# Kernel tuning notes

Hardware: AMD Instinct MI355X
Metric: run time of the kernel (lower is better)

Reference implementation:

```python
import jax, jax.numpy as jnp
import numpy as np

B, S, D_IN, D_H = 16, 4096, 512, 512

def setup_inputs() -> dict:
    key = jax.random.key(0)
    ks = jax.random.split(key, 8)
    inp = {
        "input": jax.random.normal(ks[0], (B, D_IN), dtype=jnp.float32),
        "context": jax.random.normal(ks[1], (B, S, D_IN), dtype=jnp.float32),
        "mask": jax.random.bernoulli(ks[2], 0.2, (B, S)),
        # parameters (torch nn.Linear layout: W [out,in], b [out])
        "W_in": jax.random.normal(ks[3], (D_H, D_IN), dtype=jnp.float32) / np.sqrt(D_IN),
        "b_in": jax.random.normal(ks[4], (D_H,), dtype=jnp.float32) * 0.01,
        "W_ctx": jax.random.normal(ks[5], (D_H, D_IN), dtype=jnp.float32) / np.sqrt(D_IN),
        "b_ctx": jax.random.normal(ks[6], (D_H,), dtype=jnp.float32) * 0.01,
        "v": jax.random.normal(ks[7], (D_H,), dtype=jnp.float32),
    }
    return inp


def reference(input, context, mask, W_in, b_in, W_ctx, b_ctx, v):
    # inp: [B, H] projected decoder state
    inp = input @ W_in.T + b_in
    # ctx: [B, S, H] projected context (this is what the torch code matmuls
    # with the softmax weights, i.e. hidden lives in hidden_dim space)
    ctx = context @ W_ctx.T + b_ctx
    # additive (Bahdanau) scores: v . tanh(inp + ctx) -> [B, S]
    scores = jnp.einsum("h,bsh->bs", v, jnp.tanh(inp[:, None, :] + ctx))
    # masked positions get -inf so they receive zero softmax weight
    scores = jnp.where(mask, -jnp.inf, scores)
    attn = jax.nn.softmax(scores, axis=-1)  # [B, S]
    # weighted sum of projected context: [B, H]
    hidden = jnp.einsum("bsh,bs->bh", ctx, attn)
    return hidden, attn
```

## Files before the change

kernel.cpp:

```cpp
#include <hip/hip_runtime.h>
#include <hip/hip_bf16.h>

#define B_  16
#define S_  4096
#define DIN 512
#define DH  512

typedef _Float16 f16x8 __attribute__((ext_vector_type(8)));
typedef float    f32x4 __attribute__((ext_vector_type(4)));


__device__ __forceinline__ float fast_tanh(float x) {
    float e = __expf(2.f * x);
    return 1.f - 2.f * __builtin_amdgcn_rcpf(e + 1.f);
}

__device__ __forceinline__ void gload_lds16(const void* g, void* l) {
    __builtin_amdgcn_global_load_lds(
        (const __attribute__((address_space(1))) void*)g,
        (__attribute__((address_space(3))) void*)l, 16, 0, 0);
}

__device__ __forceinline__ int mask_at(const void* mask, int isByte, int idx) {
    return isByte ? (int)((const unsigned char*)mask)[idx]
                  : ((const int*)mask)[idx];
}

__global__ __launch_bounds__(256)
void prep_kernel(const float* __restrict__ input,
                 const float* __restrict__ W_in,
                 const float* __restrict__ b_in,
                 const float* __restrict__ W_ctx,
                 const float* __restrict__ b_ctx,
                 const void*  __restrict__ mask,
                 _Float16* __restrict__ W16,
                 float* __restrict__ addv,
                 float* __restrict__ wsum,
                 int* __restrict__ maskflag) {
    int blk = blockIdx.x;
    int tid = threadIdx.x;
    if (blk < 256) {
        int base = blk * 1024 + tid * 4;
        float4 wv = *(const float4*)(W_ctx + base);
        union { _Float16 f[4]; ushort4 u; } cv;
        cv.f[0] = (_Float16)wv.x; cv.f[1] = (_Float16)wv.y;
        cv.f[2] = (_Float16)wv.z; cv.f[3] = (_Float16)wv.w;
        *(ushort4*)(W16 + base) = cv.u;
    } else if (blk < 288) {
        int t = blk - 256;
        int b = t >> 1;
        int h = ((t & 1) << 8) + tid;
        __shared__ float inrow[DIN];
        inrow[tid]       = input[b * DIN + tid];
        inrow[tid + 256] = input[b * DIN + tid + 256];
        __syncthreads();
        const float* wr = W_in + (size_t)h * DIN;
        float acc = 0.f;
        for (int k = 0; k < DIN; k += 4) {
            float4 w4 = *(const float4*)(wr + k);
            acc += w4.x * inrow[k] + w4.y * inrow[k + 1]
                 + w4.z * inrow[k + 2] + w4.w * inrow[k + 3];
        }
        addv[b * DH + h] = acc + b_in[h] + b_ctx[h];
    } else if (blk == 288) {
        const uint4* m4 = (const uint4*)mask;
        unsigned int orw = 0;
#pragma unroll
        for (int it = 0; it < 16; ++it) {
            uint4 w = m4[it * 256 + tid];
            orw |= (w.x | w.y | w.z | w.w);
        }
        int found = ((orw & 0xFFFFFF00u) != 0) ? 1 : 0;
        __shared__ int f;
        if (tid == 0) f = 0;
        __syncthreads();
        if (found) atomicOr(&f, 1);
        __syncthreads();
        if (tid == 0) maskflag[0] = f;
    } else {
        int base = (blk - 289) * 4096;
#pragma unroll
        for (int it = 0; it < 16; ++it)
            wsum[base + it * 256 + tid] = 0.f;
    }
}

__global__ __launch_bounds__(512, 1)
void score_kernel(const float* __restrict__ context,
                  const _Float16* __restrict__ W16,
                  const float* __restrict__ addv,
                  const float* __restrict__ v,
                  float* __restrict__ scores) {
    __shared__ __align__(16) _Float16 As[2][4096];
    __shared__ __align__(16) _Float16 Bs[2][16384];

    const int tid  = threadIdx.x;
    const int wave = tid >> 6;
    const int lane = tid & 63;
    const int l15  = lane & 15;
    const int q    = lane >> 4;
    const int sg   = wave >> 2;
    const int ng   = wave & 3;

    const int b  = blockIdx.x >> 5;
    const int st = blockIdx.x & 31;
    const int s0 = st * 128;

    const float* ctxA = context + ((size_t)b * S_ + s0) * DIN;

    const int rowA = ((tid >> 6) * 16) + (tid & 15);
    const int kbA  = ((tid >> 4) & 3) * 8;

#define STAGE_B(kc_, buf_)                                                     \
    {                                                                          \
        _Pragma("unroll")                                                      \
        for (int u = 0; u < 4; ++u) {                                          \
            int jn = wave * 4 + u;                                             \
            const _Float16* gp = W16 +                                         \
                (size_t)(jn * 16 + l15) * DIN + (kc_) * 32 + q * 8;            \
            gload_lds16(gp, &Bs[buf_][jn * 512]);                              \
        }                                                                      \
    }

#define LOADA(kc_, set_)                                                       \
    {                                                                          \
        const float* g0 = ctxA + (size_t)rowA * DIN + (kc_) * 32 + kbA;        \
        set_[0] = *(const float4*)g0;                                          \
        set_[1] = *(const float4*)(g0 + 4);                                    \
    }

#define WRITEA(set_, buf_)                                                     \
    {                                                                          \
        f16x8 h0;                                                              \
        h0[0] = (_Float16)set_[0].x; h0[1] = (_Float16)set_[0].y;              \
        h0[2] = (_Float16)set_[0].z; h0[3] = (_Float16)set_[0].w;              \
        h0[4] = (_Float16)set_[1].x; h0[5] = (_Float16)set_[1].y;              \
        h0[6] = (_Float16)set_[1].z; h0[7] = (_Float16)set_[1].w;              \
        *(f16x8*)&As[buf_][tid * 8] = h0;                                      \
    }

    f32x4 acc[4][8];
#pragma unroll
    for (int jm = 0; jm < 4; ++jm)
#pragma unroll
        for (int jn = 0; jn < 8; ++jn) acc[jm][jn] = (f32x4){0.f, 0.f, 0.f, 0.f};

    float4 aA[2], aB[2];

    STAGE_B(0, 0);
    LOADA(0, aA);
    WRITEA(aA, 0);
    LOADA(1, aB);
    __syncthreads();

#define STEP(kc_, buf_, ldset_, wrset_)                                        \
    {                                                                          \
        if ((kc_) + 1 < 16) STAGE_B((kc_) + 1, (buf_) ^ 1);                    \
        if ((kc_) + 2 < 16) LOADA((kc_) + 2, ldset_);                          \
        f16x8 afr[4], bfr[8];                                                  \
        _Pragma("unroll")                                                      \
        for (int jm = 0; jm < 4; ++jm)                                         \
            afr[jm] = *(const f16x8*)&As[buf_][(sg * 4 + jm) * 512 +           \
                                              q * 128 + l15 * 8];              \
        _Pragma("unroll")                                                      \
        for (int jn = 0; jn < 8; ++jn)                                         \
            bfr[jn] = *(const f16x8*)&Bs[buf_][(ng * 8 + jn) * 512 +           \
                                              q * 128 + l15 * 8];              \
        _Pragma("unroll")                                                      \
        for (int jn = 0; jn < 8; ++jn)                                         \
            _Pragma("unroll")                                                  \
            for (int jm = 0; jm < 4; ++jm)                                     \
                acc[jm][jn] = __builtin_amdgcn_mfma_f32_16x16x32_f16(          \
                    afr[jm], bfr[jn], acc[jm][jn], 0, 0, 0);                   \
        if ((kc_) + 1 < 16) WRITEA(wrset_, (buf_) ^ 1);                        \
        __syncthreads();                                                       \
    }

    for (int kp = 0; kp < 8; ++kp) {
        STEP(2 * kp,     0, aA, aB);
        STEP(2 * kp + 1, 1, aB, aA);
    }

    const float* avb = addv + b * DH;
    float rowsum[4][4] = {{0.f,0.f,0.f,0.f},{0.f,0.f,0.f,0.f},
                          {0.f,0.f,0.f,0.f},{0.f,0.f,0.f,0.f}};
#pragma unroll
    for (int jn = 0; jn < 8; ++jn) {
        int n = (ng * 8 + jn) * 16 + l15;
        float av = avb[n];
        float vv = v[n];
#pragma unroll
        for (int jm = 0; jm < 4; ++jm)
#pragma unroll
            for (int r = 0; r < 4; ++r)
                rowsum[jm][r] += vv * fast_tanh(acc[jm][jn][r] + av);
    }
    float* sredF = (float*)&As[0][0];
#pragma unroll
    for (int jm = 0; jm < 4; ++jm)
#pragma unroll
        for (int r = 0; r < 4; ++r) {
            float s = rowsum[jm][r];
            s += __shfl_xor(s, 1, 16);
            s += __shfl_xor(s, 2, 16);
            s += __shfl_xor(s, 4, 16);
            s += __shfl_xor(s, 8, 16);
            if (l15 == 0) {
                int rowL = (sg * 4 + jm) * 16 + q * 4 + r;
                sredF[ng * 128 + rowL] = s;
            }
        }
    __syncthreads();
    if (tid < 128) {
        float out = sredF[tid] + sredF[128 + tid] +
                    sredF[256 + tid] + sredF[384 + tid];
        scores[b * S_ + s0 + tid] = out;
    }
}

__global__ __launch_bounds__(256)
void attnwsum_kernel(const float* __restrict__ scores,
                     const float* __restrict__ context,
                     const void* __restrict__ mask,
                     const int* __restrict__ maskflag,
                     float* __restrict__ attn,
                     float* __restrict__ wsum) {
    __shared__ float rbuf[8];
    __shared__ int   selIdx[64];
    __shared__ float selW[64];
    __shared__ int   selCount;

    int b  = blockIdx.x >> 6;
    int c0 = (blockIdx.x & 63) * 64;
    int tid = threadIdx.x;
    int wv = tid >> 6, ln = tid & 63;
    int isByte = maskflag[0];
    const float* sr = scores + b * S_;

    float mx = -__builtin_inff();
    float vals[16];
#pragma unroll
    for (int it = 0; it < 16; ++it) {
        int s = it * 256 + tid;
        float x = mask_at(mask, isByte, b * S_ + s) ? -__builtin_inff() : sr[s];
        vals[it] = x;
        mx = fmaxf(mx, x);
    }
    for (int o = 1; o < 64; o <<= 1) mx = fmaxf(mx, __shfl_xor(mx, o, 64));
    if (ln == 0) rbuf[wv] = mx;
    __syncthreads();
    mx = fmaxf(fmaxf(rbuf[0], rbuf[1]), fmaxf(rbuf[2], rbuf[3]));

    float sum = 0.f;
#pragma unroll
    for (int it = 0; it < 16; ++it) sum += __expf(vals[it] - mx);
    for (int o = 1; o < 64; o <<= 1) sum += __shfl_xor(sum, o, 64);
    if (ln == 0) rbuf[4 + wv] = sum;
    if (tid == 0) selCount = 0;
    __syncthreads();
    float inv = 1.f / (rbuf[4] + rbuf[5] + rbuf[6] + rbuf[7]);

    if (tid < 64) {
        int s = c0 + tid;
        int idx = b * S_ + s;
        float sc = mask_at(mask, isByte, idx) ? -__builtin_inff() : sr[s];
        float p = __expf(sc - mx) * inv;
        attn[idx] = p;
        if (p > 1e-9f) {
            int k = atomicAdd(&selCount, 1);
            selIdx[k] = s;
            selW[k]  = p;
        }
    }
    __syncthreads();

    int cnt = selCount;
    if (cnt == 0) return;
    const float* cb = context + (size_t)b * S_ * DIN;
    float a00 = 0.f, a01 = 0.f, a10 = 0.f, a11 = 0.f;
    float a20 = 0.f, a21 = 0.f, a30 = 0.f, a31 = 0.f;
    int i = 0;
    for (; i + 4 <= cnt; i += 4) {
        const float* c0p = cb + (size_t)selIdx[i]     * DIN;
        const float* c1p = cb + (size_t)selIdx[i + 1] * DIN;
        const float* c2p = cb + (size_t)selIdx[i + 2] * DIN;
        const float* c3p = cb + (size_t)selIdx[i + 3] * DIN;
        float w0 = selW[i], w1 = selW[i + 1], w2 = selW[i + 2], w3 = selW[i + 3];
        a00 += w0 * c0p[tid]; a01 += w0 * c0p[tid + 256];
        a10 += w1 * c1p[tid]; a11 += w1 * c1p[tid + 256];
        a20 += w2 * c2p[tid]; a21 += w2 * c2p[tid + 256];
        a30 += w3 * c3p[tid]; a31 += w3 * c3p[tid + 256];
    }
    float acc0 = (a00 + a10) + (a20 + a30);
    float acc1 = (a01 + a11) + (a21 + a31);
    for (; i < cnt; ++i) {
        const float* cr = cb + (size_t)selIdx[i] * DIN;
        float w = selW[i];
        acc0 += w * cr[tid];
        acc1 += w * cr[tid + 256];
    }
    atomicAdd(&wsum[b * DIN + tid], acc0);
    atomicAdd(&wsum[b * DIN + tid + 256], acc1);
}

__global__ __launch_bounds__(256)
void hidden_kernel(const float* __restrict__ W_ctx,
                   const float* __restrict__ b_ctx,
                   const float* __restrict__ wsum,
                   float* __restrict__ hidden) {
    int b = blockIdx.x >> 1;
    int tid = threadIdx.x;
    int h = ((blockIdx.x & 1) << 8) + tid;
    __shared__ float wrow[DIN];
    wrow[tid]       = wsum[b * DIN + tid];
    wrow[tid + 256] = wsum[b * DIN + tid + 256];
    __syncthreads();
    const float* wr = W_ctx + (size_t)h * DIN;
    float acc = 0.f;
    for (int k = 0; k < DIN; k += 4) {
        float4 w4 = *(const float4*)(wr + k);
        acc += w4.x * wrow[k] + w4.y * wrow[k + 1]
             + w4.z * wrow[k + 2] + w4.w * wrow[k + 3];
    }
    hidden[b * DH + h] = acc + b_ctx[h];
}

extern "C" void kernel_launch(void* const* d_in, const int* in_sizes, int n_in,
                              void* d_out, int out_size, void* d_ws, size_t ws_size,
                              hipStream_t stream) {
    const float* input   = (const float*)d_in[0];
    const float* context = (const float*)d_in[1];
    const void*  mask    = d_in[2];
    const float* W_in    = (const float*)d_in[3];
    const float* b_in    = (const float*)d_in[4];
    const float* W_ctx   = (const float*)d_in[5];
    const float* b_ctx   = (const float*)d_in[6];
    const float* v       = (const float*)d_in[7];

    char* ws = (char*)d_ws;
    _Float16* W16   = (_Float16*)ws;
    float* addv     = (float*)(ws + 524288);
    float* scores   = (float*)(ws + 557056);
    float* wsum     = (float*)(ws + 819200);
    int*   maskflag = (int*)(ws + 851968);

    float* hidden = (float*)d_out;
    float* attn   = (float*)d_out + B_ * DH;

    prep_kernel<<<291, 256, 0, stream>>>(input, W_in, b_in, W_ctx, b_ctx, mask,
                                         W16, addv, wsum, maskflag);
    score_kernel<<<512, 512, 0, stream>>>(context, W16, addv, v, scores);
    attnwsum_kernel<<<B_ * 64, 256, 0, stream>>>(scores, context, mask, maskflag,
                                                 attn, wsum);
    hidden_kernel<<<B_ * 2, 256, 0, stream>>>(W_ctx, b_ctx, wsum, hidden);
}
```

Measured before the change: 290.4 us.

## Double score kernel waves to 1024 threads with halved per-wave row tiles

Launches the score GEMM with 16 waves per block instead of 8. Each wave now owns two 16-row M tiles instead of four, and context loading and W staging are re-split so each thread handles half as much. The aim is more waves in flight to hide global load latency on the context stream, plus lower per-wave register use. The cost is more LDS reads of B fragments, since each one is now shared by twice as many waves, and heavier barriers with 1024 threads.

```diff
diff --git a/kernel.cpp b/kernel.cpp
--- a/kernel.cpp
+++ b/kernel.cpp
@@ -7,6 +7,7 @@
 #define DH  512
 
 typedef _Float16 f16x8 __attribute__((ext_vector_type(8)));
+typedef _Float16 f16x4 __attribute__((ext_vector_type(4)));
 typedef float    f32x4 __attribute__((ext_vector_type(4)));
 
 
@@ -85,7 +86,7 @@
     }
 }
 
-__global__ __launch_bounds__(512, 1)
+__global__ __launch_bounds__(1024)
 void score_kernel(const float* __restrict__ context,
                   const _Float16* __restrict__ W16,
                   const float* __restrict__ addv,
@@ -108,14 +109,14 @@
 
     const float* ctxA = context + ((size_t)b * S_ + s0) * DIN;
 
-    const int rowA = ((tid >> 6) * 16) + (tid & 15);
-    const int kbA  = ((tid >> 4) & 3) * 8;
+    const int rowA = ((tid >> 7) * 16) + ((tid >> 1) & 15);
+    const int kbA  = (((tid >> 5) & 3) * 8) + ((tid & 1) * 4);
 
 #define STAGE_B(kc_, buf_)                                                     \
     {                                                                          \
         _Pragma("unroll")                                                      \
-        for (int u = 0; u < 4; ++u) {                                          \
-            int jn = wave * 4 + u;                                             \
+        for (int u = 0; u < 2; ++u) {                                          \
+            int jn = wave * 2 + u;                                             \
             const _Float16* gp = W16 +                                         \
                 (size_t)(jn * 16 + l15) * DIN + (kc_) * 32 + q * 8;            \
             gload_lds16(gp, &Bs[buf_][jn * 512]);                              \
@@ -124,28 +125,24 @@
 
 #define LOADA(kc_, set_)                                                       \
     {                                                                          \
-        const float* g0 = ctxA + (size_t)rowA * DIN + (kc_) * 32 + kbA;        \
-        set_[0] = *(const float4*)g0;                                          \
-        set_[1] = *(const float4*)(g0 + 4);                                    \
+        set_ = *(const float4*)(ctxA + (size_t)rowA * DIN + (kc_) * 32 + kbA); \
     }
 
 #define WRITEA(set_, buf_)                                                     \
     {                                                                          \
-        f16x8 h0;                                                              \
-        h0[0] = (_Float16)set_[0].x; h0[1] = (_Float16)set_[0].y;              \
-        h0[2] = (_Float16)set_[0].z; h0[3] = (_Float16)set_[0].w;              \
-        h0[4] = (_Float16)set_[1].x; h0[5] = (_Float16)set_[1].y;              \
-        h0[6] = (_Float16)set_[1].z; h0[7] = (_Float16)set_[1].w;              \
-        *(f16x8*)&As[buf_][tid * 8] = h0;                                      \
-    }
-
-    f32x4 acc[4][8];
-#pragma unroll
-    for (int jm = 0; jm < 4; ++jm)
+        f16x4 h0;                                                              \
+        h0[0] = (_Float16)set_.x; h0[1] = (_Float16)set_.y;                    \
+        h0[2] = (_Float16)set_.z; h0[3] = (_Float16)set_.w;                    \
+        *(f16x4*)&As[buf_][tid * 4] = h0;                                      \
+    }
+
+    f32x4 acc[2][8];
+#pragma unroll
+    for (int jm = 0; jm < 2; ++jm)
 #pragma unroll
         for (int jn = 0; jn < 8; ++jn) acc[jm][jn] = (f32x4){0.f, 0.f, 0.f, 0.f};
 
-    float4 aA[2], aB[2];
+    float4 aA, aB;
 
     STAGE_B(0, 0);
     LOADA(0, aA);
@@ -157,21 +154,20 @@
     {                                                                          \
         if ((kc_) + 1 < 16) STAGE_B((kc_) + 1, (buf_) ^ 1);                    \
         if ((kc_) + 2 < 16) LOADA((kc_) + 2, ldset_);                          \
-        f16x8 afr[4], bfr[8];                                                  \
+        f16x8 afr[2];                                                          \
         _Pragma("unroll")                                                      \
-        for (int jm = 0; jm < 4; ++jm)                                         \
-            afr[jm] = *(const f16x8*)&As[buf_][(sg * 4 + jm) * 512 +           \
+        for (int jm = 0; jm < 2; ++jm)                                         \
+            afr[jm] = *(const f16x8*)&As[buf_][(sg * 2 + jm) * 512 +           \
                                               q * 128 + l15 * 8];              \
         _Pragma("unroll")                                                      \
-        for (int jn = 0; jn < 8; ++jn)                                         \
-            bfr[jn] = *(const f16x8*)&Bs[buf_][(ng * 8 + jn) * 512 +           \
-                                              q * 128 + l15 * 8];              \
-        _Pragma("unroll")                                                      \
-        for (int jn = 0; jn < 8; ++jn)                                         \
-            _Pragma("unroll")                                                  \
-            for (int jm = 0; jm < 4; ++jm)                                     \
-                acc[jm][jn] = __builtin_amdgcn_mfma_f32_16x16x32_f16(          \
-                    afr[jm], bfr[jn], acc[jm][jn], 0, 0, 0);                   \
+        for (int jn = 0; jn < 8; ++jn) {                                       \
+            f16x8 bfr = *(const f16x8*)&Bs[buf_][(ng * 8 + jn) * 512 +         \
+                                                q * 128 + l15 * 8];            \
+            acc[0][jn] = __builtin_amdgcn_mfma_f32_16x16x32_f16(               \
+                afr[0], bfr, acc[0][jn], 0, 0, 0);                             \
+            acc[1][jn] = __builtin_amdgcn_mfma_f32_16x16x32_f16(               \
+                afr[1], bfr, acc[1][jn], 0, 0, 0);                             \
+        }                                                                      \
         if ((kc_) + 1 < 16) WRITEA(wrset_, (buf_) ^ 1);                        \
         __syncthreads();                                                       \
     }
@@ -182,22 +178,21 @@
     }
 
     const float* avb = addv + b * DH;
-    float rowsum[4][4] = {{0.f,0.f,0.f,0.f},{0.f,0.f,0.f,0.f},
-                          {0.f,0.f,0.f,0.f},{0.f,0.f,0.f,0.f}};
+    float rowsum[2][4] = {{0.f,0.f,0.f,0.f},{0.f,0.f,0.f,0.f}};
 #pragma unroll
     for (int jn = 0; jn < 8; ++jn) {
         int n = (ng * 8 + jn) * 16 + l15;
         float av = avb[n];
         float vv = v[n];
 #pragma unroll
-        for (int jm = 0; jm < 4; ++jm)
+        for (int jm = 0; jm < 2; ++jm)
 #pragma unroll
             for (int r = 0; r < 4; ++r)
                 rowsum[jm][r] += vv * fast_tanh(acc[jm][jn][r] + av);
     }
     float* sredF = (float*)&As[0][0];
 #pragma unroll
-    for (int jm = 0; jm < 4; ++jm)
+    for (int jm = 0; jm < 2; ++jm)
 #pragma unroll
         for (int r = 0; r < 4; ++r) {
             float s = rowsum[jm][r];
@@ -206,7 +201,7 @@
             s += __shfl_xor(s, 4, 16);
             s += __shfl_xor(s, 8, 16);
             if (l15 == 0) {
-                int rowL = (sg * 4 + jm) * 16 + q * 4 + r;
+                int rowL = (sg * 2 + jm) * 16 + q * 4 + r;
                 sredF[ng * 128 + rowL] = s;
             }
         }
@@ -349,7 +344,7 @@
 
     prep_kernel<<<291, 256, 0, stream>>>(input, W_in, b_in, W_ctx, b_ctx, mask,
                                          W16, addv, wsum, maskflag);
-    score_kernel<<<512, 512, 0, stream>>>(context, W16, addv, v, scores);
+    score_kernel<<<512, 1024, 0, stream>>>(context, W16, addv, v, scores);
     attnwsum_kernel<<<B_ * 64, 256, 0, stream>>>(scores, context, mask, maskflag,
                                                  attn, wsum);
     hidden_kernel<<<B_ * 2, 256, 0, stream>>>(W_ctx, b_ctx, wsum, hidden);
```

Result: slower. 298.4 us (+2.8%).
